# Performance work log

Measured on AMD Instinct MI355X. Metric: run time of the kernel, lower is better.

Reference implementation:

```python
import jax, jax.numpy as jnp
from jax import lax
import numpy as np

B, T, E, D, OUT = 512, 128, 256, 256, 1

def setup_inputs() -> dict:
    key = jax.random.key(0)
    ks = jax.random.split(key, 16)
    s = lambda *sh: 1.0 / np.sqrt(sh[-1])
    inp = {
        "input_encoded": jax.random.normal(ks[0], (B, T, E), jnp.float32),
        "y_history": jax.random.normal(ks[1], (B, T, OUT), jnp.float32),
        # attn_layer: Linear(2D+E -> E), Tanh, Linear(E -> 1). Stored input-major [in, out].
        "aW1": jax.random.normal(ks[2], (2 * D + E, E), jnp.float32) * (1.0 / np.sqrt(2 * D + E)),
        "ab1": jnp.zeros((E,), jnp.float32),
        "aW2": jax.random.normal(ks[3], (E, 1), jnp.float32) * (1.0 / np.sqrt(E)),
        "ab2": jnp.zeros((1,), jnp.float32),
        # LSTM cell (input_size=OUT, hidden=D), torch gate order i,f,g,o; weights [4D, in]
        "Wih": jax.random.normal(ks[4], (4 * D, OUT), jnp.float32) * (1.0 / np.sqrt(D)),
        "Whh": jax.random.normal(ks[5], (4 * D, D), jnp.float32) * (1.0 / np.sqrt(D)),
        "bih": jnp.zeros((4 * D,), jnp.float32),
        "bhh": jnp.zeros((4 * D,), jnp.float32),
        # fc: Linear(E+OUT -> OUT), weight init normal_() per source
        "fcW": jax.random.normal(ks[6], (OUT, E + OUT), jnp.float32),
        "fcb": jnp.zeros((OUT,), jnp.float32),
        # fc_final: Linear(D+E -> OUT)
        "ffW": jax.random.normal(ks[7], (OUT, D + E), jnp.float32) * (1.0 / np.sqrt(D + E)),
        "ffb": jnp.zeros((OUT,), jnp.float32),
    }
    return inp

def _decoder(input_encoded, y_history, aW1, ab1, aW2, ab2, Wih, Whh, bih, bhh, fcW, fcb, ffW, ffb):
    b, t, e = input_encoded.shape
    d = Whh.shape[1]
    # Precompute the encoder part of the attention projection once: [b, t, e_hid]
    enc_proj = jnp.einsum('bte,ef->btf', input_encoded, aW1[2 * d:])

    def step(carry, y_t):
        h, c, _ = carry                                  # h,c: [b, d]
        hc = jnp.concatenate([h, c], axis=-1)            # [b, 2d]
        z = jnp.tanh(jnp.einsum('bk,kf->bf', hc, aW1[:2 * d])[:, None, :] + enc_proj + ab1)
        scores = jnp.einsum('btf,f->bt', z, aW2[:, 0]) + ab2[0]
        attn = jax.nn.softmax(scores, axis=1)            # [b, t]
        ctx = jnp.einsum('bt,bte->be', attn, input_encoded)  # [b, e]
        y_tilde = jnp.concatenate([ctx, y_t], axis=-1) @ fcW.T + fcb  # [b, out]
        gates = y_tilde @ Wih.T + h @ Whh.T + (bih + bhh)  # [b, 4d]
        i, f, g, o = jnp.split(gates, 4, axis=-1)
        c2 = jax.nn.sigmoid(f) * c + jax.nn.sigmoid(i) * jnp.tanh(g)
        h2 = jax.nn.sigmoid(o) * jnp.tanh(c2)
        return (h2, c2, ctx), None

    init = (jnp.zeros((b, d), input_encoded.dtype),
            jnp.zeros((b, d), input_encoded.dtype),
            jnp.zeros((b, e), input_encoded.dtype))
    (h, c, ctx), _ = lax.scan(step, init, jnp.swapaxes(y_history, 0, 1))
    return jnp.concatenate([h, ctx], axis=-1) @ ffW.T + ffb  # [b, out]

def reference(input_encoded, y_history, aW1, ab1, aW2, ab2, Wih, Whh, bih, bhh, fcW, fcb, ffW, ffb):
    return _decoder(input_encoded, y_history, aW1, ab1, aW2, ab2, Wih, Whh, bih, bhh, fcW, fcb, ffW, ffb)
```

## Files before the change

kernel.cpp:

```cpp
#include <hip/hip_runtime.h>


#define BB 512
#define TT 128
#define EE 256
#define DD 256
#define NB 2
#define NTHR 1024

typedef _Float16 h2 __attribute__((ext_vector_type(2)));
typedef _Float16 h8 __attribute__((ext_vector_type(8)));

#if defined(__has_builtin)
#if __has_builtin(__builtin_amdgcn_fdot2)
#define HAS_FDOT2 1
#endif
#endif

#ifdef HAS_FDOT2
#define FDOT2(a, b, c) __builtin_amdgcn_fdot2(__builtin_bit_cast(h2, (a)), __builtin_bit_cast(h2, (b)), (c), false)
#else
static __device__ __forceinline__ float FDOT2(unsigned int a, unsigned int b, float c) {
    h2 x = __builtin_bit_cast(h2, a), y = __builtin_bit_cast(h2, b);
    return c + (float)x[0] * (float)y[0] + (float)x[1] * (float)y[1];
}
#endif

static __device__ __forceinline__ float dot8u4(uint4 w, uint4 h, float acc) {
    acc = FDOT2(w.x, h.x, acc);
    acc = FDOT2(w.y, h.y, acc);
    acc = FDOT2(w.z, h.z, acc);
    acc = FDOT2(w.w, h.w, acc);
    return acc;
}
static __device__ __forceinline__ unsigned int pkh(float a, float b) {
    union { _Float16 h; unsigned short s; } ua, ub;
    ua.h = (_Float16)a; ub.h = (_Float16)b;
    return (unsigned int)ua.s | ((unsigned int)ub.s << 16);
}
__device__ __forceinline__ float ftanh(float x) {
    return 1.f - 2.f * __builtin_amdgcn_rcpf(__expf(2.f * x) + 1.f);
}
__device__ __forceinline__ float fsig(float x) {
    return __builtin_amdgcn_rcpf(1.f + __expf(-x));
}

__global__ __launch_bounds__(256) void k_pack(const float* __restrict__ aW1,
                                              const float* __restrict__ Whh,
                                              const float* __restrict__ bih,
                                              const float* __restrict__ bhh,
                                              _Float16* __restrict__ aW1h,
                                              _Float16* __restrict__ WhhH,
                                              float* __restrict__ bias) {
    int bid = blockIdx.x, tid = threadIdx.x;
    if (bid < 512) {
        int o = bid * 256 + tid;
        int g = o >> 11, f = (o >> 3) & 255, j = o & 7;
        aW1h[o] = (_Float16)aW1[(g * 8 + j) * EE + f];
    } else if (bid < 1536) {
        int o = (bid - 512) * 256 + tid;
        int i = o >> 13, jj = (o >> 3) & 1023, m = o & 7;
        WhhH[o] = (_Float16)Whh[jj * DD + i * 8 + m];
    } else {
        int j = (bid - 1536) * 256 + tid;
        bias[j] = bih[j] + bhh[j];
    }
}

__global__ __launch_bounds__(256) void k_encproj(const float* __restrict__ ie,
                                                 const float* __restrict__ aW1,
                                                 const float* __restrict__ fcW,
                                                 const float* __restrict__ ffW,
                                                 _Float16* __restrict__ ep,
                                                 float* __restrict__ iefc,
                                                 float* __restrict__ ieff) {
    __shared__ float a[32][EE];
    int row0 = blockIdx.x * 32;
    int tid = threadIdx.x;
    for (int r = 0; r < 32; ++r)
        a[r][tid] = ie[(size_t)(row0 + r) * EE + tid];
    __syncthreads();
    float acc[32];
    #pragma unroll
    for (int r = 0; r < 32; ++r) acc[r] = 0.f;
    const float* wenc = aW1 + 512 * EE;
    for (int e = 0; e < EE; e += 4) {
        float w0 = wenc[(e + 0) * EE + tid];
        float w1 = wenc[(e + 1) * EE + tid];
        float w2 = wenc[(e + 2) * EE + tid];
        float w3 = wenc[(e + 3) * EE + tid];
        #pragma unroll
        for (int r = 0; r < 32; ++r) {
            float4 av = *(const float4*)&a[r][e];
            acc[r] += av.x * w0 + av.y * w1 + av.z * w2 + av.w * w3;
        }
    }
    for (int r = 0; r < 32; ++r)
        ep[(size_t)(row0 + r) * EE + tid] = (_Float16)acc[r];

    int wave = tid >> 6, lane = tid & 63;
    float4 f1 = *(const float4*)&fcW[lane * 4];
    float4 f2 = *(const float4*)&ffW[EE + lane * 4];
    #pragma unroll
    for (int rr = 0; rr < 8; ++rr) {
        int r = wave * 8 + rr;
        float4 v = *(const float4*)&a[r][lane * 4];
        float p1 = v.x * f1.x + v.y * f1.y + v.z * f1.z + v.w * f1.w;
        float p2 = v.x * f2.x + v.y * f2.y + v.z * f2.z + v.w * f2.w;
        #pragma unroll
        for (int off = 1; off <= 32; off <<= 1) {
            p1 += __shfl_xor(p1, off);
            p2 += __shfl_xor(p2, off);
        }
        if (lane == 0) {
            iefc[row0 + r] = p1;
            ieff[row0 + r] = p2;
        }
    }
}

__global__ __launch_bounds__(NTHR) void k_main(
    const _Float16* __restrict__ ep, const float* __restrict__ yh,
    const _Float16* __restrict__ aW1h, const _Float16* __restrict__ WhhH,
    const float* __restrict__ bias_, const float* __restrict__ ab1,
    const float* __restrict__ aW2, const float* __restrict__ Wih,
    const float* __restrict__ fcW, const float* __restrict__ fcb,
    const float* __restrict__ ffW, const float* __restrict__ ffb,
    const float* __restrict__ iefc, const float* __restrict__ ieff,
    float* __restrict__ out) {
    __shared__ _Float16 s_ep[NB * TT * EE];
    __shared__ unsigned int s_hc16[NB][2][128];
    __shared__ float s_qp[2][NB][EE];
    __shared__ float s_sc[NB * TT];
    __shared__ float s_g[NB][4 * DD];
    __shared__ float s_wih[4 * DD];
    __shared__ float s_iefc[NB][TT];
    __shared__ float s_ieff[NB][TT];
    __shared__ float s_yh[NB][TT];
    __shared__ float s_yt[NB];
    __shared__ float s_ofs[NB];

    const int tid = threadIdx.x;
    const int wave = tid >> 6, lane = tid & 63;
    const int b0 = blockIdx.x * NB;

    {
        const uint4* src = (const uint4*)(ep + (size_t)b0 * TT * EE);
        uint4* dst = (uint4*)s_ep;
        #pragma unroll
        for (int i = 0; i < (NB * TT * EE) / 8 / NTHR; ++i)
            dst[tid + i * NTHR] = src[tid + i * NTHR];
    }
    for (int i = tid; i < 4 * DD; i += NTHR) s_wih[i] = Wih[i];
    for (int i = tid; i < NB * TT; i += NTHR) {
        int b = i >> 7, t = i & 127;
        s_iefc[b][t] = iefc[(b0 + b) * TT + t];
        s_ieff[b][t] = ieff[(b0 + b) * TT + t];
        s_yh[b][t]   = yh[(size_t)(b0 + b) * TT + t];
    }
    for (int i = tid; i < NB * 2 * 128; i += NTHR) (&s_hc16[0][0][0])[i] = 0u;

    const int qf = tid & 255, qkh = (tid >> 8) & 1, qb = tid >> 9;
    const float qinit = qkh ? 0.f : ab1[qf];
    const uint4* qW = (const uint4*)aW1h + ((size_t)(qkh * 32) * 256 + qf);
    const int qperm = 32 * (qf & 7) + (qf >> 3);

    const uint4* wP = (const uint4*)WhhH + tid;
    const float biasv = bias_[tid];

    const int l5 = lane & 31;
    const int rsub = wave * 2 + (lane >> 5);
    const int e0 = l5 * 8;
    float tw2[8]; float sw2 = 0.f;
    #pragma unroll
    for (int j = 0; j < 8; ++j) { float w = aW2[e0 + j]; tw2[j] = 2.f * w; sw2 += w; }

    const float fcw256 = fcW[256], fcb0 = fcb[0], ffb0 = ffb[0];
    float c_reg = 0.f;

    __syncthreads();

    for (int t = 0; t < TT; ++t) {
        float qa = qinit;
        float g0 = biasv, g1 = biasv;
        #pragma unroll 8
        for (int i = 0; i < 32; ++i) {
            uint4 wv = qW[(size_t)i * 256];
            uint4 hv = *(const uint4*)&s_hc16[qb][qkh][i * 4];
            qa = dot8u4(wv, hv, qa);
            uint4 gw = wP[(size_t)i * 1024];
            uint4 h0 = *(const uint4*)&s_hc16[0][0][i * 4];
            uint4 h1 = *(const uint4*)&s_hc16[1][0][i * 4];
            g0 = dot8u4(gw, h0, g0);
            g1 = dot8u4(gw, h1, g1);
        }
        s_qp[qkh][qb][qperm] = qa;
        s_g[0][tid] = g0;
        s_g[1][tid] = g1;
        __syncthreads();

        #pragma unroll
        for (int b = 0; b < NB; ++b) {
            float qs[8];
            #pragma unroll
            for (int j = 0; j < 8; ++j)
                qs[j] = 2.f * (s_qp[0][b][l5 + 32 * j] + s_qp[1][b][l5 + 32 * j]);
            const _Float16* eph = s_ep + b * TT * EE + e0;
            #pragma unroll
            for (int sw = 0; sw < 4; ++sw) {
                int tt2 = sw * 32 + rsub;
                h8 xv = *(const h8*)(eph + tt2 * EE);
                float s = sw2;
                #pragma unroll
                for (int j = 0; j < 8; ++j) {
                    float e = __expf(__fmaf_rn((float)xv[j], 2.f, qs[j]));
                    s = __fmaf_rn(-tw2[j], __builtin_amdgcn_rcpf(e + 1.f), s);
                }
                #pragma unroll
                for (int off = 1; off <= 16; off <<= 1) s += __shfl_xor(s, off);
                if (l5 == 0) s_sc[b * TT + tt2] = s;
            }
        }
        __syncthreads();

        if ((wave & 7) == 0) {
            int b = wave >> 3;
            float v0 = s_sc[b * TT + lane], v1 = s_sc[b * TT + 64 + lane];
            float m = fmaxf(v0, v1);
            #pragma unroll
            for (int off = 1; off <= 32; off <<= 1) m = fmaxf(m, __shfl_xor(m, off));
            float x0 = __expf(v0 - m), x1 = __expf(v1 - m);
            float ss = x0 + x1;
            #pragma unroll
            for (int off = 1; off <= 32; off <<= 1) ss += __shfl_xor(ss, off);
            float inv = __builtin_amdgcn_rcpf(ss);
            float a0 = x0 * inv, a1 = x1 * inv;
            float p  = a0 * s_iefc[b][lane] + a1 * s_iefc[b][64 + lane];
            float pf = (t == TT - 1) ? (a0 * s_ieff[b][lane] + a1 * s_ieff[b][64 + lane]) : 0.f;
            #pragma unroll
            for (int off = 1; off <= 32; off <<= 1) {
                p  += __shfl_xor(p, off);
                pf += __shfl_xor(pf, off);
            }
            if (lane == 0) {
                s_yt[b] = p + s_yh[b][t] * fcw256 + fcb0;
                if (t == TT - 1) s_ofs[b] = pf;
            }
        }
        __syncthreads();

        if (tid < NB * DD) {
            int b = tid >> 8, d = tid & 255;
            float yt = s_yt[b];
            float gi = s_g[b][d]          + yt * s_wih[d];
            float gf = s_g[b][DD + d]     + yt * s_wih[DD + d];
            float gg = s_g[b][2 * DD + d] + yt * s_wih[2 * DD + d];
            float go = s_g[b][3 * DD + d] + yt * s_wih[3 * DD + d];
            float c2 = fsig(gf) * c_reg + fsig(gi) * ftanh(gg);
            c_reg = c2;
            float hn = fsig(go) * ftanh(c2);
            float hO = __shfl_xor(hn, 1);
            float cO = __shfl_xor(c2, 1);
            if (!(d & 1)) {
                s_hc16[b][0][d >> 1] = pkh(hn, hO);
                s_hc16[b][1][d >> 1] = pkh(c2, cO);
            }
        }
        __syncthreads();
    }

    if ((wave & 7) == 0) {
        int b = wave >> 3;
        unsigned int p0 = s_hc16[b][0][lane * 2];
        unsigned int p1 = s_hc16[b][0][lane * 2 + 1];
        h2 ha = __builtin_bit_cast(h2, p0), hb = __builtin_bit_cast(h2, p1);
        float4 w = *(const float4*)&ffW[lane * 4];
        float p = (float)ha[0] * w.x + (float)ha[1] * w.y
                + (float)hb[0] * w.z + (float)hb[1] * w.w;
        #pragma unroll
        for (int off = 1; off <= 32; off <<= 1) p += __shfl_xor(p, off);
        if (lane == 0) out[b0 + b] = p + s_ofs[b] + ffb0;
    }
}

extern "C" void kernel_launch(void* const* d_in, const int* in_sizes, int n_in,
                              void* d_out, int out_size, void* d_ws, size_t ws_size,
                              hipStream_t stream) {
    const float* ie  = (const float*)d_in[0];
    const float* yh  = (const float*)d_in[1];
    const float* aW1 = (const float*)d_in[2];
    const float* ab1 = (const float*)d_in[3];
    const float* aW2 = (const float*)d_in[4];
    const float* Wih = (const float*)d_in[6];
    const float* Whh = (const float*)d_in[7];
    const float* bih = (const float*)d_in[8];
    const float* bhh = (const float*)d_in[9];
    const float* fcW = (const float*)d_in[10];
    const float* fcb = (const float*)d_in[11];
    const float* ffW = (const float*)d_in[12];
    const float* ffb = (const float*)d_in[13];
    float* out = (float*)d_out;

    _Float16* ep   = (_Float16*)d_ws;
    _Float16* aW1h = ep + (size_t)BB * TT * EE;
    _Float16* WhhH = aW1h + 512 * EE;
    float* bias = (float*)(WhhH + 262144);
    float* iefc = bias + 1024;
    float* ieff = iefc + BB * TT;

    k_pack<<<1540, 256, 0, stream>>>(aW1, Whh, bih, bhh, aW1h, WhhH, bias);
    k_encproj<<<2048, 256, 0, stream>>>(ie, aW1, fcW, ffW, ep, iefc, ieff);
    k_main<<<BB / NB, NTHR, 0, stream>>>(ep, yh, aW1h, WhhH, bias, ab1, aW2,
                                         Wih, fcW, fcb, ffW, ffb, iefc, ieff, out);
}
```

Before: 2.026 ms.

## Process one batch row per 512-thread block and merge softmax with LSTM update

Switches k_main from two batch rows per 1024-thread block to one row per 512-thread block, launching 512 blocks instead of 256. Each thread now computes two gate outputs, and the attention projection takes h or c depending on its half. The softmax/context step and the LSTM cell update are merged into one phase, which removes one block barrier per timestep, and the final offset is kept in a register. The goal is more blocks in flight (launch bounds request 4 per CU), shorter critical-path barriers and lower shared memory per block. In exchange, each block now reads Whh/aW1 weights for only one row, which roughly doubles the weight traffic per batch row.

New measurement: 2.129 ms. 5.1% more time.

```diff
diff --git a/kernel.cpp b/kernel.cpp
--- a/kernel.cpp
+++ b/kernel.cpp
@@ -5,8 +5,7 @@
 #define TT 128
 #define EE 256
 #define DD 256
-#define NB 2
-#define NTHR 1024
+#define NTHR 512
 
 typedef _Float16 h2 __attribute__((ext_vector_type(2)));
 typedef _Float16 h8 __attribute__((ext_vector_type(8)));
@@ -119,7 +118,7 @@
     }
 }
 
-__global__ __launch_bounds__(NTHR) void k_main(
+__global__ __launch_bounds__(NTHR, 4) void k_main(
     const _Float16* __restrict__ ep, const float* __restrict__ yh,
     const _Float16* __restrict__ aW1h, const _Float16* __restrict__ WhhH,
     const float* __restrict__ bias_, const float* __restrict__ ab1,
@@ -128,45 +127,43 @@
     const float* __restrict__ ffW, const float* __restrict__ ffb,
     const float* __restrict__ iefc, const float* __restrict__ ieff,
     float* __restrict__ out) {
-    __shared__ _Float16 s_ep[NB * TT * EE];
-    __shared__ unsigned int s_hc16[NB][2][128];
-    __shared__ float s_qp[2][NB][EE];
-    __shared__ float s_sc[NB * TT];
-    __shared__ float s_g[NB][4 * DD];
+    __shared__ _Float16 s_ep[TT * EE];
+    __shared__ unsigned int s_hc16[2][128];
+    __shared__ float s_qp[2][EE];
+    __shared__ float s_sc[TT];
+    __shared__ float s_g[4 * DD];
     __shared__ float s_wih[4 * DD];
-    __shared__ float s_iefc[NB][TT];
-    __shared__ float s_ieff[NB][TT];
-    __shared__ float s_yh[NB][TT];
-    __shared__ float s_yt[NB];
-    __shared__ float s_ofs[NB];
+    __shared__ float s_iefc[TT];
+    __shared__ float s_ieff[TT];
+    __shared__ float s_yh[TT];
 
     const int tid = threadIdx.x;
     const int wave = tid >> 6, lane = tid & 63;
-    const int b0 = blockIdx.x * NB;
+    const int b0 = blockIdx.x;
 
     {
         const uint4* src = (const uint4*)(ep + (size_t)b0 * TT * EE);
         uint4* dst = (uint4*)s_ep;
         #pragma unroll
-        for (int i = 0; i < (NB * TT * EE) / 8 / NTHR; ++i)
+        for (int i = 0; i < (TT * EE) / 8 / NTHR; ++i)
             dst[tid + i * NTHR] = src[tid + i * NTHR];
     }
     for (int i = tid; i < 4 * DD; i += NTHR) s_wih[i] = Wih[i];
-    for (int i = tid; i < NB * TT; i += NTHR) {
-        int b = i >> 7, t = i & 127;
-        s_iefc[b][t] = iefc[(b0 + b) * TT + t];
-        s_ieff[b][t] = ieff[(b0 + b) * TT + t];
-        s_yh[b][t]   = yh[(size_t)(b0 + b) * TT + t];
-    }
-    for (int i = tid; i < NB * 2 * 128; i += NTHR) (&s_hc16[0][0][0])[i] = 0u;
-
-    const int qf = tid & 255, qkh = (tid >> 8) & 1, qb = tid >> 9;
+    if (tid < TT) {
+        s_iefc[tid] = iefc[b0 * TT + tid];
+        s_ieff[tid] = ieff[b0 * TT + tid];
+        s_yh[tid]   = yh[(size_t)b0 * TT + tid];
+    }
+    if (tid < 256) (&s_hc16[0][0])[tid] = 0u;
+
+    const int qf = tid & 255, qkh = tid >> 8;
     const float qinit = qkh ? 0.f : ab1[qf];
     const uint4* qW = (const uint4*)aW1h + ((size_t)(qkh * 32) * 256 + qf);
     const int qperm = 32 * (qf & 7) + (qf >> 3);
 
-    const uint4* wP = (const uint4*)WhhH + tid;
-    const float biasv = bias_[tid];
+    const uint4* wPa = (const uint4*)WhhH + tid;
+    const uint4* wPb = (const uint4*)WhhH + tid + 512;
+    const float bias_a = bias_[tid], bias_b = bias_[tid + 512];
 
     const int l5 = lane & 31;
     const int rsub = wave * 2 + (lane >> 5);
@@ -177,38 +174,39 @@
 
     const float fcw256 = fcW[256], fcb0 = fcb[0], ffb0 = ffb[0];
     float c_reg = 0.f;
+    float ofs_reg = 0.f;
 
     __syncthreads();
 
     for (int t = 0; t < TT; ++t) {
         float qa = qinit;
-        float g0 = biasv, g1 = biasv;
+        float g0 = bias_a, g1 = bias_b;
         #pragma unroll 8
         for (int i = 0; i < 32; ++i) {
-            uint4 wv = qW[(size_t)i * 256];
-            uint4 hv = *(const uint4*)&s_hc16[qb][qkh][i * 4];
-            qa = dot8u4(wv, hv, qa);
-            uint4 gw = wP[(size_t)i * 1024];
-            uint4 h0 = *(const uint4*)&s_hc16[0][0][i * 4];
-            uint4 h1 = *(const uint4*)&s_hc16[1][0][i * 4];
-            g0 = dot8u4(gw, h0, g0);
-            g1 = dot8u4(gw, h1, g1);
-        }
-        s_qp[qkh][qb][qperm] = qa;
-        s_g[0][tid] = g0;
-        s_g[1][tid] = g1;
+            uint4 wq = qW[(size_t)i * 256];
+            uint4 wa = wPa[(size_t)i * 1024];
+            uint4 wb = wPb[(size_t)i * 1024];
+            uint4 hv = *(const uint4*)&s_hc16[0][i * 4];
+            uint4 cv = *(const uint4*)&s_hc16[1][i * 4];
+            uint4 hq = qkh ? cv : hv;
+            qa = dot8u4(wq, hq, qa);
+            g0 = dot8u4(wa, hv, g0);
+            g1 = dot8u4(wb, hv, g1);
+        }
+        s_qp[qkh][qperm] = qa;
+        s_g[tid] = g0;
+        s_g[tid + 512] = g1;
         __syncthreads();
 
-        #pragma unroll
-        for (int b = 0; b < NB; ++b) {
+        {
             float qs[8];
             #pragma unroll
             for (int j = 0; j < 8; ++j)
-                qs[j] = 2.f * (s_qp[0][b][l5 + 32 * j] + s_qp[1][b][l5 + 32 * j]);
-            const _Float16* eph = s_ep + b * TT * EE + e0;
-            #pragma unroll
-            for (int sw = 0; sw < 4; ++sw) {
-                int tt2 = sw * 32 + rsub;
+                qs[j] = 2.f * (s_qp[0][l5 + 32 * j] + s_qp[1][l5 + 32 * j]);
+            const _Float16* eph = s_ep + e0;
+            #pragma unroll
+            for (int sw = 0; sw < 8; ++sw) {
+                int tt2 = sw * 16 + rsub;
                 h8 xv = *(const h8*)(eph + tt2 * EE);
                 float s = sw2;
                 #pragma unroll
@@ -218,14 +216,13 @@
                 }
                 #pragma unroll
                 for (int off = 1; off <= 16; off <<= 1) s += __shfl_xor(s, off);
-                if (l5 == 0) s_sc[b * TT + tt2] = s;
+                if (l5 == 0) s_sc[tt2] = s;
             }
         }
         __syncthreads();
 
-        if ((wave & 7) == 0) {
-            int b = wave >> 3;
-            float v0 = s_sc[b * TT + lane], v1 = s_sc[b * TT + 64 + lane];
+        {
+            float v0 = s_sc[lane], v1 = s_sc[64 + lane];
             float m = fmaxf(v0, v1);
             #pragma unroll
             for (int off = 1; off <= 32; off <<= 1) m = fmaxf(m, __shfl_xor(m, off));
@@ -235,51 +232,46 @@
             for (int off = 1; off <= 32; off <<= 1) ss += __shfl_xor(ss, off);
             float inv = __builtin_amdgcn_rcpf(ss);
             float a0 = x0 * inv, a1 = x1 * inv;
-            float p  = a0 * s_iefc[b][lane] + a1 * s_iefc[b][64 + lane];
-            float pf = (t == TT - 1) ? (a0 * s_ieff[b][lane] + a1 * s_ieff[b][64 + lane]) : 0.f;
-            #pragma unroll
-            for (int off = 1; off <= 32; off <<= 1) {
-                p  += __shfl_xor(p, off);
-                pf += __shfl_xor(pf, off);
+            float p = a0 * s_iefc[lane] + a1 * s_iefc[64 + lane];
+            #pragma unroll
+            for (int off = 1; off <= 32; off <<= 1) p += __shfl_xor(p, off);
+            float yt = p + s_yh[t] * fcw256 + fcb0;
+            if (t == TT - 1) {
+                float pf = a0 * s_ieff[lane] + a1 * s_ieff[64 + lane];
+                #pragma unroll
+                for (int off = 1; off <= 32; off <<= 1) pf += __shfl_xor(pf, off);
+                ofs_reg = pf;
             }
-            if (lane == 0) {
-                s_yt[b] = p + s_yh[b][t] * fcw256 + fcb0;
-                if (t == TT - 1) s_ofs[b] = pf;
+            if (tid < DD) {
+                int d = tid;
+                float gi = s_g[d]          + yt * s_wih[d];
+                float gf = s_g[DD + d]     + yt * s_wih[DD + d];
+                float gg = s_g[2 * DD + d] + yt * s_wih[2 * DD + d];
+                float go = s_g[3 * DD + d] + yt * s_wih[3 * DD + d];
+                float c2 = fsig(gf) * c_reg + fsig(gi) * ftanh(gg);
+                c_reg = c2;
+                float hn = fsig(go) * ftanh(c2);
+                float hO = __shfl_xor(hn, 1);
+                float cO = __shfl_xor(c2, 1);
+                if (!(d & 1)) {
+                    s_hc16[0][d >> 1] = pkh(hn, hO);
+                    s_hc16[1][d >> 1] = pkh(c2, cO);
+                }
             }
         }
         __syncthreads();
-
-        if (tid < NB * DD) {
-            int b = tid >> 8, d = tid & 255;
-            float yt = s_yt[b];
-            float gi = s_g[b][d]          + yt * s_wih[d];
-            float gf = s_g[b][DD + d]     + yt * s_wih[DD + d];
-            float gg = s_g[b][2 * DD + d] + yt * s_wih[2 * DD + d];
-            float go = s_g[b][3 * DD + d] + yt * s_wih[3 * DD + d];
-            float c2 = fsig(gf) * c_reg + fsig(gi) * ftanh(gg);
-            c_reg = c2;
-            float hn = fsig(go) * ftanh(c2);
-            float hO = __shfl_xor(hn, 1);
-            float cO = __shfl_xor(c2, 1);
-            if (!(d & 1)) {
-                s_hc16[b][0][d >> 1] = pkh(hn, hO);
-                s_hc16[b][1][d >> 1] = pkh(c2, cO);
-            }
-        }
-        __syncthreads();
-    }
-
-    if ((wave & 7) == 0) {
-        int b = wave >> 3;
-        unsigned int p0 = s_hc16[b][0][lane * 2];
-        unsigned int p1 = s_hc16[b][0][lane * 2 + 1];
+    }
+
+    if (wave == 0) {
+        unsigned int p0 = s_hc16[0][lane * 2];
+        unsigned int p1 = s_hc16[0][lane * 2 + 1];
         h2 ha = __builtin_bit_cast(h2, p0), hb = __builtin_bit_cast(h2, p1);
         float4 w = *(const float4*)&ffW[lane * 4];
         float p = (float)ha[0] * w.x + (float)ha[1] * w.y
                 + (float)hb[0] * w.z + (float)hb[1] * w.w;
         #pragma unroll
         for (int off = 1; off <= 32; off <<= 1) p += __shfl_xor(p, off);
-        if (lane == 0) out[b0 + b] = p + s_ofs[b] + ffb0;
+        if (lane == 0) out[b0] = p + ofs_reg + ffb0;
     }
 }
 
@@ -310,6 +302,6 @@
 
     k_pack<<<1540, 256, 0, stream>>>(aW1, Whh, bih, bhh, aW1h, WhhH, bias);
     k_encproj<<<2048, 256, 0, stream>>>(ie, aW1, fcW, ffW, ep, iefc, ieff);
-    k_main<<<BB / NB, NTHR, 0, stream>>>(ep, yh, aW1h, WhhH, bias, ab1, aW2,
-                                         Wih, fcW, fcb, ffW, ffb, iefc, ieff, out);
-}
+    k_main<<<BB, NTHR, 0, stream>>>(ep, yh, aW1h, WhhH, bias, ab1, aW2,
+                                    Wih, fcW, fcb, ffW, ffb, iefc, ieff, out);
+}
```
